# Kernel tuning notes

Hardware: AMD Instinct MI355X
Metric: run time of the kernel (lower is better)

Reference implementation:

```python
import jax, jax.numpy as jnp
import numpy as np

H, C = 4, 64            # heads, channels per head (graph_hidden_channels)
GHC = H * C             # concat width = 256
FIN = 32                # num_node_features
NHID = 256
NOUT = 256
NEG_SLOPE = 0.2         # PyG GATConv default negative_slope


def gat_conv(x, src, dst, n, W, a_src, a_dst, bias):
    # x: [N, Fin], W: [Fin, H*C], a_src/a_dst: [H, C], bias: [H*C]
    h = (x @ W).reshape(n, H, C)                       # [N,H,C]
    s = (h * a_src).sum(-1)                            # [N,H] src logits
    d = (h * a_dst).sum(-1)                            # [N,H] dst logits
    e = jax.nn.leaky_relu(s[src] + d[dst], NEG_SLOPE)  # [E,H]
    m = jax.ops.segment_max(e, dst, num_segments=n)    # segment softmax (stable)
    ex = jnp.exp(e - m[dst])
    denom = jax.ops.segment_sum(ex, dst, num_segments=n)
    alpha = ex / jnp.maximum(denom[dst], 1e-16)        # [E,H]
    msg = h[src] * alpha[:, :, None]                   # [E,H,C]
    out = jax.ops.segment_sum(msg, dst, num_segments=n)
    return out.reshape(n, GHC) + bias


def setup_inputs() -> dict:
    key = jax.random.key(0)
    ks = jax.random.split(key, 32)
    N, E, G = 50000, 800000, 256
    inp = {
        'x': jax.random.normal(ks[0], (N, FIN), dtype=jnp.float32),
        'edge_index': jax.random.randint(ks[1], (2, E), 0, N, dtype=jnp.int32),
        'batch': jnp.sort(jax.random.randint(ks[2], (N,), 0, G, dtype=jnp.int32)),
        'num_graphs': G,
    }
    def p(k, shape):
        return jax.random.normal(k, shape, dtype=jnp.float32) * 0.05
    # three GATConv layers + head linears
    ins = [FIN, C, C]
    i = 3
    for l, fin in enumerate(ins, start=1):
        inp[f'W{l}'] = p(ks[i], (fin, GHC)); i += 1
        inp[f'a{l}s'] = p(ks[i], (H, C)); i += 1
        inp[f'a{l}d'] = p(ks[i], (H, C)); i += 1
        inp[f'b{l}'] = p(ks[i], (GHC,)); i += 1
        inp[f'hl{l}_w'] = p(ks[i], (GHC, C)); i += 1
        inp[f'hl{l}_b'] = p(ks[i], (C,)); i += 1
    inp['mh1_w'] = p(ks[i], (C, NHID)); i += 1
    inp['mh1_b'] = p(ks[i], (NHID,)); i += 1
    inp['mh2_w'] = p(ks[i], (NHID, NOUT)); i += 1
    inp['mh2_b'] = p(ks[i], (NOUT,))
    return inp


def reference(x, edge_index, batch, num_graphs,
              W1, a1s, a1d, b1, hl1_w, hl1_b,
              W2, a2s, a2d, b2, hl2_w, hl2_b,
              W3, a3s, a3d, b3, hl3_w, hl3_b,
              mh1_w, mh1_b, mh2_w, mh2_b):
    n = x.shape[0]
    loops = jnp.arange(n, dtype=edge_index.dtype)  # PyG add_self_loops=True
    src = jnp.concatenate([edge_index[0], loops])
    dst = jnp.concatenate([edge_index[1], loops])

    h = gat_conv(x, src, dst, n, W1, a1s, a1d, b1)
    h = jax.nn.relu(h @ hl1_w + hl1_b)
    h = gat_conv(h, src, dst, n, W2, a2s, a2d, b2)
    h = jax.nn.relu(h @ hl2_w + hl2_b)
    h = gat_conv(h, src, dst, n, W3, a3s, a3d, b3)
    h = h @ hl3_w + hl3_b                      # no relu before pooling (as in source)

    sums = jax.ops.segment_sum(h, batch, num_segments=num_graphs)
    cnt = jax.ops.segment_sum(jnp.ones((n,), h.dtype), batch, num_segments=num_graphs)
    g = sums / jnp.maximum(cnt, 1.0)[:, None]  # global_mean_pool

    g = jax.nn.relu(g @ mh1_w + mh1_b)
    return g @ mh2_w + mh2_b
```

## Files before the change

kernel.cpp:

```cpp
#include <hip/hip_runtime.h>
#include <hip/hip_bf16.h>
#include <hip/hip_fp16.h>
#include <math.h>

#define HD 4
#define CH 64
#define GHC 256
#define NEG 0.2f
#define CHUNK 4096
#define BCAP 16384

#define WAVE_SYNC() do { __builtin_amdgcn_wave_barrier(); \
                         asm volatile("s_waitcnt lgkmcnt(0)" ::: "memory"); } while (0)

typedef _Float16 f16x8 __attribute__((ext_vector_type(8)));
typedef float f32x4 __attribute__((ext_vector_type(4)));

__device__ __forceinline__ float wsum32(float v){
  #pragma unroll
  for (int o = 16; o > 0; o >>= 1) v += __shfl_xor(v, o);
  return v;
}

__global__ __launch_bounds__(256)
void bin_stage(const int* __restrict__ ei, int E, int N,
               int* __restrict__ bres, unsigned* __restrict__ pairs)
{
  __shared__ unsigned staged[CHUNK];
  __shared__ unsigned short bkt[CHUNK];
  __shared__ int cnts[256], loff[256], gpos[256];
  const int t = threadIdx.x;
  const int tot = E + N;
  const int cbase = blockIdx.x * CHUNK;
  if (cbase >= tot) return;

  cnts[t] = 0;
  __syncthreads();

  unsigned myp[CHUNK / 256];
  int myb[CHUNK / 256], myr[CHUNK / 256];
  #pragma unroll
  for (int j = 0; j < CHUNK / 256; j++){
    int i = cbase + t + j * 256;
    myb[j] = -1;
    if (i < tot){
      int src, dst;
      if (i < E){ src = ei[i]; dst = ei[E + i]; }
      else { src = dst = i - E; }
      myb[j] = dst >> 8;
      myp[j] = (unsigned)src | ((unsigned)dst << 16);
      myr[j] = atomicAdd(&cnts[myb[j]], 1);
    }
  }
  __syncthreads();

  int v = cnts[t];
  loff[t] = v;
  __syncthreads();
  for (int o = 1; o < 256; o <<= 1){
    int tv = (t >= o) ? loff[t - o] : 0;
    __syncthreads();
    loff[t] += tv;
    __syncthreads();
  }
  int excl = loff[t] - v;
  __syncthreads();
  loff[t] = excl;
  __syncthreads();

  #pragma unroll
  for (int j = 0; j < CHUNK / 256; j++){
    if (myb[j] >= 0){
      int slot = loff[myb[j]] + myr[j];
      staged[slot] = myp[j];
      bkt[slot] = (unsigned short)myb[j];
    }
  }
  if (v > 0) gpos[t] = atomicAdd(&bres[t], v);
  __syncthreads();

  int total = min(CHUNK, tot - cbase);
  for (int i = t; i < total; i += 256){
    int b = bkt[i];
    int addr = b * BCAP + gpos[b] + (i - loff[b]);
    pairs[addr] = staged[i];
  }
}

__global__ __launch_bounds__(256)
void build_csr(const unsigned* __restrict__ pairs, const int* __restrict__ bres,
               int N, int Etot, int* __restrict__ offs, unsigned short* __restrict__ csr)
{
  __shared__ int dcnt[256], doff[256], bscan[256];
  const int b = blockIdx.x, t = threadIdx.x;
  int bv = bres[t];
  bscan[t] = bv;
  __syncthreads();
  for (int o = 1; o < 256; o <<= 1){
    int tv = (t >= o) ? bscan[t - o] : 0;
    __syncthreads();
    bscan[t] += tv;
    __syncthreads();
  }
  const int beg = bscan[b] - bres[b];
  const int cnt = bres[b];
  const unsigned* pb = pairs + (size_t)b * BCAP;
  dcnt[t] = 0;
  __syncthreads();
  for (int i = t; i < cnt; i += 256)
    atomicAdd(&dcnt[(pb[i] >> 16) & 255], 1);
  __syncthreads();
  int v = dcnt[t];
  doff[t] = v;
  __syncthreads();
  for (int o = 1; o < 256; o <<= 1){
    int tv = (t >= o) ? doff[t - o] : 0;
    __syncthreads();
    doff[t] += tv;
    __syncthreads();
  }
  int excl = doff[t] - v;
  __syncthreads();
  doff[t] = excl;
  __syncthreads();
  int node = (b << 8) + t;
  if (node < N) offs[node] = beg + doff[t];
  if (b == 0 && t == 0) offs[N] = Etot;
  dcnt[t] = 0;
  __syncthreads();
  for (int i = t; i < cnt; i += 256){
    unsigned pr = pb[i];
    int l = (pr >> 16) & 255;
    int pos = beg + doff[l] + atomicAdd(&dcnt[l], 1);
    csr[pos] = (unsigned short)(pr & 0xFFFF);
  }
}

__global__ __launch_bounds__(256)
void fuse_all(const float* __restrict__ W1, const float* __restrict__ a1s,
              const float* __restrict__ a1d, const float* __restrict__ b1,
              const float* __restrict__ h1w, const float* __restrict__ h1b,
              const float* __restrict__ W2, const float* __restrict__ a2s,
              const float* __restrict__ a2d, const float* __restrict__ b2,
              const float* __restrict__ h2w, const float* __restrict__ h2b,
              const float* __restrict__ W3, const float* __restrict__ a3s,
              const float* __restrict__ a3d, const float* __restrict__ b3,
              const float* __restrict__ h3w, const float* __restrict__ h3b,
              __half* __restrict__ Wpk1, float* __restrict__ Psd1, float* __restrict__ cb1,
              __half* __restrict__ Wpk2, __half* __restrict__ Ppk2, float* __restrict__ cb2,
              float* __restrict__ Wcp3, __half* __restrict__ Ppk3, float* __restrict__ cb3,
              const int* __restrict__ batch, int N, int G, int* __restrict__ bnd)
{
  const int blk = blockIdx.x, t = threadIdx.x;
  if (blk >= 163){
    int g = (blk - 163) * 256 + t;
    if (g > G) return;
    if (g == G){ bnd[G] = N; return; }
    int lo = 0, hi = N;
    while (lo < hi){ int mid = (lo + hi) >> 1; if (batch[mid] < g) lo = mid + 1; else hi = mid; }
    bnd[g] = lo;
    return;
  }
  const float *W, *as, *ad, *bl, *hlw, *hlb;
  float *cb;
  int FIN, b, layer;
  if (blk < 33){
    W = W1; as = a1s; ad = a1d; bl = b1; hlw = h1w; hlb = h1b;
    cb = cb1; FIN = 32; b = blk; layer = 1;
  } else if (blk < 98){
    W = W2; as = a2s; ad = a2d; bl = b2; hlw = h2w; hlb = h2b;
    cb = cb2; FIN = 64; b = blk - 33; layer = 2;
  } else {
    W = W3; as = a3s; ad = a3d; bl = b3; hlw = h3w; hlb = h3b;
    cb = cb3; FIN = 64; b = blk - 98; layer = 3;
  }
  if (b < FIN){
    const int c = t >> 2, h = t & 3;
    const float* wrow = W + b * GHC + h * 64;
    float acc = 0.f;
    #pragma unroll 8
    for (int j = 0; j < 64; j++)
      acc += wrow[j] * hlw[(h * 64 + j) * CH + c];
    const int k = h * FIN + b;
    if (layer == 3){
      Wcp3[k * CH + c] = acc;
    } else {
      int ks = k >> 5, nt = c >> 4;
      int lane = (((k & 31) >> 3) << 4) | (c & 15);
      int idx = ((ks * 4 + nt) * 64 + lane) * 8 + (k & 7);
      __half* Wpk = (layer == 1) ? Wpk1 : Wpk2;
      Wpk[idx] = __float2half(acc);
    }
    if (t < 8){
      const int hh = t & 3;
      const float* a = (t < 4) ? as : ad;
      const float* wr2 = W + b * GHC + hh * 64;
      float p = 0.f;
      #pragma unroll 8
      for (int j = 0; j < 64; j++) p += wr2[j] * a[hh * 64 + j];
      if (layer == 1){
        Psd1[b * 8 + t] = p;
      } else {
        int kk = b;
        int ks = kk >> 5;
        int lane = (((kk & 31) >> 3) << 4) | t;
        int idx = (ks * 64 + lane) * 8 + (kk & 7);
        __half* Ppk = (layer == 2) ? Ppk2 : Ppk3;
        Ppk[idx] = __float2half(p);
      }
    }
  } else if (t < CH){
    float acc = hlb[t];
    for (int j = 0; j < GHC; j++) acc += bl[j] * hlw[j * CH + t];
    cb[t] = acc;
  }
}

__global__ __launch_bounds__(256)
void logits_from_x(const float* __restrict__ x, const float* __restrict__ Psd,
                   float* __restrict__ s_log, float* __restrict__ d_log,
                   __half* __restrict__ xh0, int N)
{
  int idx = blockIdx.x * 256 + threadIdx.x;
  int node = idx >> 3, q = idx & 7;
  if (node >= N) return;
  const float* xr = x + (size_t)node * 32;
  float v = 0.f;
  #pragma unroll 8
  for (int k = 0; k < 32; k++) v += xr[k] * Psd[k * 8 + q];
  if (q < 4){
    s_log[node * 4 + q] = v;
    __half2 h0 = __floats2half2_rn(xr[q*8+0], xr[q*8+1]);
    __half2 h1 = __floats2half2_rn(xr[q*8+2], xr[q*8+3]);
    __half2 h2 = __floats2half2_rn(xr[q*8+4], xr[q*8+5]);
    __half2 h3 = __floats2half2_rn(xr[q*8+6], xr[q*8+7]);
    uint4 u;
    u.x = *reinterpret_cast<const unsigned*>(&h0);
    u.y = *reinterpret_cast<const unsigned*>(&h1);
    u.z = *reinterpret_cast<const unsigned*>(&h2);
    u.w = *reinterpret_cast<const unsigned*>(&h3);
    *reinterpret_cast<uint4*>(xh0 + (size_t)node * 32 + q * 8) = u;
  } else {
    d_log[node * 4 + (q - 4)] = v;
  }
}

template<int F, int ZW>
__global__ __launch_bounds__(512)
void gat_layer_fused(const __half* __restrict__ xin, const float* __restrict__ s_in,
                     const float* __restrict__ d_in_, const int* __restrict__ off,
                     const unsigned short* __restrict__ csr,
                     const __half* __restrict__ Wpk, const float* __restrict__ cb,
                     const __half* __restrict__ Ppk,
                     __half* __restrict__ xo, float* __restrict__ s_out,
                     float* __restrict__ d_out_, int N)
{
  constexpr int ZP = ZW + 8;
  __shared__ float4 qa[8][2][32];
  __shared__ int    qs[8][2][32];
  __shared__ __half z_lds[16][ZP];
  __shared__ float  outs[16][68];
  __shared__ float  cbs[64];
  const int tid  = threadIdx.x;
  const int wv   = tid >> 6;
  const int lane = tid & 63;
  const int half = lane >> 5;
  const int l32  = lane & 31;
  const int n0 = blockIdx.x * 16;
  const int n = n0 + wv * 2 + half;
  const bool valid = n < N;
  if (tid < 64) cbs[tid] = cb[tid];

  int beg = 0, deg = 0;
  if (valid){ beg = off[n]; deg = off[n + 1] - beg; }

  float d4[4] = {0.f, 0.f, 0.f, 0.f};
  if (valid){
    float4 d4v = reinterpret_cast<const float4*>(d_in_)[n];
    d4[0] = d4v.x; d4[1] = d4v.y; d4[2] = d4v.z; d4[3] = d4v.w;
  }

  float den[4], ex[4];
  int s = 0;
  {
    const bool act = valid && (l32 < deg);
    if (act){
      s = csr[beg + l32];
      float4 sl = reinterpret_cast<const float4*>(s_in)[s];
      float t[4] = {sl.x, sl.y, sl.z, sl.w};
      #pragma unroll
      for (int i = 0; i < 4; i++){
        float u = t[i] + d4[i]; u = (u >= 0.f) ? u : NEG * u;
        ex[i] = __expf(u);
      }
    } else {
      #pragma unroll
      for (int i = 0; i < 4; i++) ex[i] = 0.f;
    }
    #pragma unroll
    for (int i = 0; i < 4; i++) den[i] = wsum32(ex[i]);
  }
  for (int base = 32; base < deg; base += 32){
    const int k = base + l32;
    float e2[4] = {0.f, 0.f, 0.f, 0.f};
    if (k < deg){
      int s2 = csr[beg + k];
      float4 sl = reinterpret_cast<const float4*>(s_in)[s2];
      float t[4] = {sl.x, sl.y, sl.z, sl.w};
      #pragma unroll
      for (int i = 0; i < 4; i++){
        float u = t[i] + d4[i]; u = (u >= 0.f) ? u : NEG * u;
        e2[i] = __expf(u);
      }
    }
    #pragma unroll
    for (int i = 0; i < 4; i++) den[i] += wsum32(e2[i]);
  }

  float dninv[4];
  #pragma unroll
  for (int i = 0; i < 4; i++) dninv[i] = 1.f / fmaxf(den[i], 1e-16f);

  float a0[4] = {0.f,0.f,0.f,0.f};
  float a1[4] = {0.f,0.f,0.f,0.f};
  const float4* qap = qa[wv][half];
  const int*    qsp = qs[wv][half];

  auto accum = [&](int cnt){
    int cntR = (cnt + 3) & ~3;
    if (F == 64){
      const __half* xb = xin + 2 * l32;
      for (int e0 = 0; e0 < cntR; e0 += 4){
        float4 al[4]; int sv[4]; unsigned uv[4];
        #pragma unroll
        for (int j = 0; j < 4; j++){ al[j] = qap[e0 + j]; sv[j] = qsp[e0 + j]; }
        #pragma unroll
        for (int j = 0; j < 4; j++)
          uv[j] = *reinterpret_cast<const unsigned*>(xb + sv[j] * 64);
        #pragma unroll
        for (int j = 0; j < 4; j++){
          float2 f = __half22float2(*reinterpret_cast<const __half2*>(&uv[j]));
          a0[0] += al[j].x * f.x; a1[0] += al[j].x * f.y;
          a0[1] += al[j].y * f.x; a1[1] += al[j].y * f.y;
          a0[2] += al[j].z * f.x; a1[2] += al[j].z * f.y;
          a0[3] += al[j].w * f.x; a1[3] += al[j].w * f.y;
        }
      }
    } else {
      const __half* xb = xin + l32;
      for (int e0 = 0; e0 < cntR; e0 += 4){
        float4 al[4]; int sv[4]; __half hv[4];
        #pragma unroll
        for (int j = 0; j < 4; j++){ al[j] = qap[e0 + j]; sv[j] = qsp[e0 + j]; }
        #pragma unroll
        for (int j = 0; j < 4; j++)
          hv[j] = xb[sv[j] * 32];
        #pragma unroll
        for (int j = 0; j < 4; j++){
          float xv = __half2float(hv[j]);
          a0[0] += al[j].x * xv;
          a0[1] += al[j].y * xv;
          a0[2] += al[j].z * xv;
          a0[3] += al[j].w * xv;
        }
      }
    }
  };

  if (deg <= 32){
    qa[wv][half][l32] = make_float4(ex[0] * dninv[0], ex[1] * dninv[1],
                                    ex[2] * dninv[2], ex[3] * dninv[3]);
    qs[wv][half][l32] = s;
    WAVE_SYNC();
    accum(deg);
  } else {
    for (int base = 0; base < deg; base += 32){
      const int k = base + l32;
      int s2 = 0; float al[4] = {0.f, 0.f, 0.f, 0.f};
      if (k < deg){
        s2 = csr[beg + k];
        float4 sl = reinterpret_cast<const float4*>(s_in)[s2];
        float t[4] = {sl.x, sl.y, sl.z, sl.w};
        #pragma unroll
        for (int i = 0; i < 4; i++){
          float u = t[i] + d4[i]; u = (u >= 0.f) ? u : NEG * u;
          al[i] = __expf(u) * dninv[i];
        }
      }
      qa[wv][half][l32] = make_float4(al[0], al[1], al[2], al[3]);
      qs[wv][half][l32] = s2;
      WAVE_SYNC();
      accum(min(32, deg - base));
      WAVE_SYNC();
    }
  }

  {
    const int r = wv * 2 + half;
    if (F == 64){
      #pragma unroll
      for (int h = 0; h < 4; h++){
        __half2 hv = __floats2half2_rn(a0[h], a1[h]);
        *reinterpret_cast<unsigned*>(&z_lds[r][h * 64 + 2 * l32]) =
            *reinterpret_cast<const unsigned*>(&hv);
      }
    } else {
      #pragma unroll
      for (int h = 0; h < 4; h++)
        z_lds[r][h * 32 + l32] = __float2half(a0[h]);
    }
  }
  __syncthreads();

  const int row = lane & 15, kg = lane >> 4;
  if (wv < 4){
    const int nt = wv;
    f32x4 acc = {0.f,0.f,0.f,0.f};
    const f16x8* wp = reinterpret_cast<const f16x8*>(Wpk) + lane;
    #pragma unroll
    for (int ks = 0; ks < ZW / 32; ks++){
      f16x8 af = *reinterpret_cast<const f16x8*>(&z_lds[row][kg * 8 + ks * 32]);
      acc = __builtin_amdgcn_mfma_f32_16x16x32_f16(af, wp[(ks*4+nt)*64], acc, 0,0,0);
    }
    #pragma unroll
    for (int r = 0; r < 4; r++){
      int rr = kg * 4 + r;
      outs[rr][nt * 16 + row] = fmaxf(acc[r] + cbs[nt * 16 + row], 0.f);
    }
  }
  __syncthreads();

  if (tid < 256){
    int nn = tid >> 4, part = tid & 15;
    int node = n0 + nn;
    if (node < N){
      const float* o = &outs[nn][part * 4];
      __half2 h0 = __floats2half2_rn(o[0], o[1]);
      __half2 h1 = __floats2half2_rn(o[2], o[3]);
      uint2 u;
      u.x = *reinterpret_cast<const unsigned*>(&h0);
      u.y = *reinterpret_cast<const unsigned*>(&h1);
      *reinterpret_cast<uint2*>(xo + (size_t)node * 64 + part * 4) = u;
    }
  }

  if (wv == 4){
    f32x4 lacc = {0.f,0.f,0.f,0.f};
    const f16x8* pp = reinterpret_cast<const f16x8*>(Ppk) + lane;
    #pragma unroll
    for (int ks = 0; ks < 2; ks++){
      f16x8 af;
      #pragma unroll
      for (int j = 0; j < 8; j++) af[j] = (_Float16)outs[row][ks * 32 + kg * 8 + j];
      lacc = __builtin_amdgcn_mfma_f32_16x16x32_f16(af, pp[ks * 64], lacc, 0,0,0);
    }
    if (row < 8){
      float* dst = (row < 4) ? s_out : d_out_;
      int q = row & 3;
      #pragma unroll
      for (int r = 0; r < 4; r++){
        int node = n0 + kg * 4 + r;
        if (node < N) dst[node * 4 + q] = lacc[r];
      }
    }
  }
}

template<int F>
__global__ __launch_bounds__(256)
void gat_aggregate_z(const __half* __restrict__ xin, const float* __restrict__ s_log,
                     const float* __restrict__ d_log, const int* __restrict__ off,
                     const unsigned short* __restrict__ csr, __half* __restrict__ z, int N)
{
  __shared__ float4 qa[4][2][32];
  __shared__ int    qs[4][2][32];
  const int wv   = threadIdx.x >> 6;
  const int lane = threadIdx.x & 63;
  const int half = lane >> 5;
  const int l32  = lane & 31;
  const int n = blockIdx.x * 8 + wv * 2 + half;
  const bool valid = n < N;

  int beg = 0, deg = 0;
  if (valid){ beg = off[n]; deg = off[n + 1] - beg; }

  float d4[4] = {0.f, 0.f, 0.f, 0.f};
  if (valid){
    float4 d4v = reinterpret_cast<const float4*>(d_log)[n];
    d4[0] = d4v.x; d4[1] = d4v.y; d4[2] = d4v.z; d4[3] = d4v.w;
  }

  float den[4], ex[4];
  int s = 0;
  {
    const bool act = valid && (l32 < deg);
    if (act){
      s = csr[beg + l32];
      float4 sl = reinterpret_cast<const float4*>(s_log)[s];
      float t[4] = {sl.x, sl.y, sl.z, sl.w};
      #pragma unroll
      for (int i = 0; i < 4; i++){
        float u = t[i] + d4[i]; u = (u >= 0.f) ? u : NEG * u;
        ex[i] = __expf(u);
      }
    } else {
      #pragma unroll
      for (int i = 0; i < 4; i++) ex[i] = 0.f;
    }
    #pragma unroll
    for (int i = 0; i < 4; i++) den[i] = wsum32(ex[i]);
  }
  for (int base = 32; base < deg; base += 32){
    const int k = base + l32;
    float e2[4] = {0.f, 0.f, 0.f, 0.f};
    if (k < deg){
      int s2 = csr[beg + k];
      float4 sl = reinterpret_cast<const float4*>(s_log)[s2];
      float t[4] = {sl.x, sl.y, sl.z, sl.w};
      #pragma unroll
      for (int i = 0; i < 4; i++){
        float u = t[i] + d4[i]; u = (u >= 0.f) ? u : NEG * u;
        e2[i] = __expf(u);
      }
    }
    #pragma unroll
    for (int i = 0; i < 4; i++) den[i] += wsum32(e2[i]);
  }

  float dninv[4];
  #pragma unroll
  for (int i = 0; i < 4; i++) dninv[i] = 1.f / fmaxf(den[i], 1e-16f);

  float a0[4] = {0.f,0.f,0.f,0.f};
  float a1[4] = {0.f,0.f,0.f,0.f};
  const float4* qap = qa[wv][half];
  const int*    qsp = qs[wv][half];

  auto accum = [&](int cnt){
    int cntR = (cnt + 3) & ~3;
    const __half* xb = xin + 2 * l32;
    for (int e0 = 0; e0 < cntR; e0 += 4){
      float4 al[4]; int sv[4]; unsigned uv[4];
      #pragma unroll
      for (int j = 0; j < 4; j++){ al[j] = qap[e0 + j]; sv[j] = qsp[e0 + j]; }
      #pragma unroll
      for (int j = 0; j < 4; j++)
        uv[j] = *reinterpret_cast<const unsigned*>(xb + sv[j] * 64);
      #pragma unroll
      for (int j = 0; j < 4; j++){
        float2 f = __half22float2(*reinterpret_cast<const __half2*>(&uv[j]));
        a0[0] += al[j].x * f.x; a1[0] += al[j].x * f.y;
        a0[1] += al[j].y * f.x; a1[1] += al[j].y * f.y;
        a0[2] += al[j].z * f.x; a1[2] += al[j].z * f.y;
        a0[3] += al[j].w * f.x; a1[3] += al[j].w * f.y;
      }
    }
  };

  if (deg <= 32){
    qa[wv][half][l32] = make_float4(ex[0] * dninv[0], ex[1] * dninv[1],
                                    ex[2] * dninv[2], ex[3] * dninv[3]);
    qs[wv][half][l32] = s;
    WAVE_SYNC();
    accum(deg);
  } else {
    for (int base = 0; base < deg; base += 32){
      const int k = base + l32;
      int s2 = 0; float al[4] = {0.f, 0.f, 0.f, 0.f};
      if (k < deg){
        s2 = csr[beg + k];
        float4 sl = reinterpret_cast<const float4*>(s_log)[s2];
        float t[4] = {sl.x, sl.y, sl.z, sl.w};
        #pragma unroll
        for (int i = 0; i < 4; i++){
          float u = t[i] + d4[i]; u = (u >= 0.f) ? u : NEG * u;
          al[i] = __expf(u) * dninv[i];
        }
      }
      qa[wv][half][l32] = make_float4(al[0], al[1], al[2], al[3]);
      qs[wv][half][l32] = s2;
      WAVE_SYNC();
      accum(min(32, deg - base));
      WAVE_SYNC();
    }
  }

  if (valid){
    const size_t zb = (size_t)n * 256 + 2 * l32;
    #pragma unroll
    for (int h = 0; h < 4; h++){
      __half2 hv = __floats2half2_rn(a0[h], a1[h]);
      *reinterpret_cast<unsigned*>(z + zb + h * 64) =
          *reinterpret_cast<const unsigned*>(&hv);
    }
  }
}

__global__ __launch_bounds__(256)
void pool_partial(const __half* __restrict__ z3, const int* __restrict__ bnd,
                  float* __restrict__ psum)
{
  const int blk = blockIdx.x, tid = threadIdx.x;
  const int g = blk >> 2, part = blk & 3;
  const int s = bnd[g], e = bnd[g + 1];
  const int cp = tid & 127, rp = tid >> 7;
  float ax = 0.f, ay = 0.f;
  for (int n = s + part + 4 * rp; n < e; n += 8){
    __half2 hv = *reinterpret_cast<const __half2*>(z3 + (size_t)n * 256 + 2 * cp);
    float2 f = __half22float2(hv);
    ax += f.x; ay += f.y;
  }
  __shared__ float shx[2][128], shy[2][128];
  shx[rp][cp] = ax; shy[rp][cp] = ay;
  __syncthreads();
  if (tid < 128){
    psum[(size_t)blk * 256 + 2 * tid]     = shx[0][tid] + shx[1][tid];
    psum[(size_t)blk * 256 + 2 * tid + 1] = shy[0][tid] + shy[1][tid];
  }
}

__global__ __launch_bounds__(256)
void head_mlp(const float* __restrict__ psum, const int* __restrict__ bnd,
              const float* __restrict__ Wcp3, const float* __restrict__ cb3,
              const float* __restrict__ m1w, const float* __restrict__ m1b,
              const float* __restrict__ m2w, const float* __restrict__ m2b,
              float* __restrict__ out)
{
  const int g = blockIdx.x, tid = threadIdx.x;
  const float cnt = (float)max(bnd[g + 1] - bnd[g], 1);
  __shared__ float zbar[256];
  const float* pb = psum + (size_t)g * 1024;
  zbar[tid] = (pb[tid] + pb[256 + tid] + pb[512 + tid] + pb[768 + tid]) / cnt;
  __syncthreads();
  const int c = tid & 63, part = tid >> 6;
  float tp = 0.f;
  #pragma unroll 8
  for (int k = part * 64; k < part * 64 + 64; k++) tp += zbar[k] * Wcp3[k * 64 + c];
  __shared__ float tsh[4][64];
  tsh[part][c] = tp;
  __syncthreads();
  __shared__ float tvec[64];
  if (tid < 64)
    tvec[tid] = tsh[0][tid] + tsh[1][tid] + tsh[2][tid] + tsh[3][tid] + cb3[tid];
  __syncthreads();
  float a = m1b[tid];
  #pragma unroll 8
  for (int cc = 0; cc < 64; cc++) a += tvec[cc] * m1w[cc * 256 + tid];
  __shared__ float g1row[256];
  g1row[tid] = fmaxf(a, 0.f);
  __syncthreads();
  float o = m2b[tid];
  #pragma unroll 8
  for (int k = 0; k < 256; k++) o += g1row[k] * m2w[k * 256 + tid];
  out[g * 256 + tid] = o;
}

extern "C" void kernel_launch(void* const* d_in, const int* in_sizes, int n_in,
                              void* d_out, int out_size, void* d_ws, size_t ws_size,
                              hipStream_t stream)
{
  const float* x     = (const float*)d_in[0];
  const int*   ei    = (const int*)d_in[1];
  const int*   batch = (const int*)d_in[2];
  const float* W1  = (const float*)d_in[4];
  const float* a1s = (const float*)d_in[5];
  const float* a1d = (const float*)d_in[6];
  const float* b1  = (const float*)d_in[7];
  const float* h1w = (const float*)d_in[8];
  const float* h1b = (const float*)d_in[9];
  const float* W2  = (const float*)d_in[10];
  const float* a2s = (const float*)d_in[11];
  const float* a2d = (const float*)d_in[12];
  const float* b2  = (const float*)d_in[13];
  const float* h2w = (const float*)d_in[14];
  const float* h2b = (const float*)d_in[15];
  const float* W3  = (const float*)d_in[16];
  const float* a3s = (const float*)d_in[17];
  const float* a3d = (const float*)d_in[18];
  const float* b3  = (const float*)d_in[19];
  const float* h3w = (const float*)d_in[20];
  const float* h3b = (const float*)d_in[21];
  const float* m1w = (const float*)d_in[22];
  const float* m1b = (const float*)d_in[23];
  const float* m2w = (const float*)d_in[24];
  const float* m2b = (const float*)d_in[25];

  const int N = in_sizes[0] / 32;
  const int E = in_sizes[1] / 2;
  const int G = out_size / 256;
  const int Etot = E + N;
  const int nbuck = (N + 255) >> 8;

  char* p = (char*)d_ws;
  auto alloc = [&](size_t bytes) -> void* {
    void* r = (void*)p;
    p += ((bytes + 255) / 256) * 256;
    return r;
  };
  __half* zbuf   = (__half*)alloc((size_t)N * GHC * 2);
  __half* xh0    = (__half*)alloc((size_t)N * 32 * 2);
  __half* xh1    = (__half*)alloc((size_t)N * CH * 2);
  __half* xh2    = (__half*)alloc((size_t)N * CH * 2);
  float* s_logA  = (float*)alloc((size_t)N * HD * 4);
  float* d_logA  = (float*)alloc((size_t)N * HD * 4);
  float* s_logB  = (float*)alloc((size_t)N * HD * 4);
  float* d_logB  = (float*)alloc((size_t)N * HD * 4);
  int*   offs    = (int*)alloc((size_t)(N + 1) * 4);
  unsigned short* csr = (unsigned short*)alloc((size_t)Etot * 2);
  unsigned* pairs = (unsigned*)alloc((size_t)nbuck * BCAP * 4);
  int*    bres   = (int*)alloc(256 * 4);
  __half* Ppk2   = (__half*)alloc(1024 * 2);
  __half* Ppk3   = (__half*)alloc(1024 * 2);
  int*   bnd     = (int*)alloc((size_t)(G + 1) * 4);
  float* psum    = (float*)alloc((size_t)G * 4 * 256 * 4);
  float* Wcp3    = (float*)alloc(256 * 64 * 4);
  float* Psd1    = (float*)alloc(32 * 8 * 4);
  float* cb1     = (float*)alloc(64 * 4);
  float* cb2     = (float*)alloc(64 * 4);
  float* cb3     = (float*)alloc(64 * 4);
  __half* Wpk1   = (__half*)alloc(128 * 64 * 2);
  __half* Wpk2   = (__half*)alloc(256 * 64 * 2);

  hipMemsetAsync(bres, 0, 5120, stream);

  const int cb_blocks = (Etot + CHUNK - 1) / CHUNK;
  bin_stage<<<cb_blocks, 256, 0, stream>>>(ei, E, N, bres, pairs);
  build_csr<<<nbuck, 256, 0, stream>>>(pairs, bres, N, Etot, offs, csr);

  const int fb = 163 + (G + 256) / 256;
  fuse_all<<<fb, 256, 0, stream>>>(W1, a1s, a1d, b1, h1w, h1b,
                                   W2, a2s, a2d, b2, h2w, h2b,
                                   W3, a3s, a3d, b3, h3w, h3b,
                                   Wpk1, Psd1, cb1, Wpk2, Ppk2, cb2, Wcp3, Ppk3, cb3,
                                   batch, N, G, bnd);

  logits_from_x<<<((size_t)N * 8 + 255) / 256, 256, 0, stream>>>(x, Psd1, s_logA, d_logA, xh0, N);

  const int fgrid = (N + 15) / 16;
  gat_layer_fused<32, 128><<<fgrid, 512, 0, stream>>>(xh0, s_logA, d_logA, offs, csr,
                                                      Wpk1, cb1, Ppk2, xh1, s_logB, d_logB, N);
  gat_layer_fused<64, 256><<<fgrid, 512, 0, stream>>>(xh1, s_logB, d_logB, offs, csr,
                                                      Wpk2, cb2, Ppk3, xh2, s_logA, d_logA, N);

  const int ab = (N + 7) / 8;
  gat_aggregate_z<64><<<ab, 256, 0, stream>>>(xh2, s_logA, d_logA, offs, csr, zbuf, N);

  pool_partial<<<G * 4, 256, 0, stream>>>(zbuf, bnd, psum);
  head_mlp<<<G, 256, 0, stream>>>(psum, bnd, Wcp3, cb3, m1w, m1b, m2w, m2b, (float*)d_out);
}
```

Before: 161.7 us.

## Sort nodes by in-degree so aggregation blocks process similar-degree nodes

Adds a degree histogram in build_csr and a new perm_scatter kernel that buckets nodes by in-degree into a permutation array. The GAT layer kernels and the final aggregation then read their node ids through this permutation, so the nodes sharing a wave or block have similar degree. The aim is to cut load imbalance and idle lanes when degrees vary within a wave. The cost is an extra kernel launch, global atomics, and scattered, less coalesced writes of per-node outputs. Neighbour locality is also lost.

```diff
diff --git a/kernel.cpp b/kernel.cpp
--- a/kernel.cpp
+++ b/kernel.cpp
@@ -89,7 +89,8 @@
 
 __global__ __launch_bounds__(256)
 void build_csr(const unsigned* __restrict__ pairs, const int* __restrict__ bres,
-               int N, int Etot, int* __restrict__ offs, unsigned short* __restrict__ csr)
+               int N, int Etot, int* __restrict__ offs, unsigned short* __restrict__ csr,
+               int* __restrict__ ghist)
 {
   __shared__ int dcnt[256], doff[256], bscan[256];
   const int b = blockIdx.x, t = threadIdx.x;
@@ -124,7 +125,10 @@
   doff[t] = excl;
   __syncthreads();
   int node = (b << 8) + t;
-  if (node < N) offs[node] = beg + doff[t];
+  if (node < N){
+    offs[node] = beg + doff[t];
+    atomicAdd(&ghist[min(v, 255)], 1);
+  }
   if (b == 0 && t == 0) offs[N] = Etot;
   dcnt[t] = 0;
   __syncthreads();
@@ -133,6 +137,33 @@
     int l = (pr >> 16) & 255;
     int pos = beg + doff[l] + atomicAdd(&dcnt[l], 1);
     csr[pos] = (unsigned short)(pr & 0xFFFF);
+  }
+}
+
+__global__ __launch_bounds__(256)
+void perm_scatter(const int* __restrict__ offs, const int* __restrict__ ghist,
+                  int* __restrict__ gbincnt, int* __restrict__ perm, int N)
+{
+  __shared__ int sc[256];
+  const int t = threadIdx.x;
+  int v = ghist[t];
+  sc[t] = v;
+  __syncthreads();
+  for (int o = 1; o < 256; o <<= 1){
+    int tv = (t >= o) ? sc[t - o] : 0;
+    __syncthreads();
+    sc[t] += tv;
+    __syncthreads();
+  }
+  __shared__ int base[256];
+  base[t] = sc[t] - v;
+  __syncthreads();
+  int node = blockIdx.x * 256 + t;
+  if (node < N){
+    int deg = offs[node + 1] - offs[node];
+    int bin = min(deg, 255);
+    int pos = base[bin] + atomicAdd(&gbincnt[bin], 1);
+    perm[pos] = node;
   }
 }
 
@@ -249,7 +280,7 @@
 __global__ __launch_bounds__(512)
 void gat_layer_fused(const __half* __restrict__ xin, const float* __restrict__ s_in,
                      const float* __restrict__ d_in_, const int* __restrict__ off,
-                     const unsigned short* __restrict__ csr,
+                     const unsigned short* __restrict__ csr, const int* __restrict__ perm,
                      const __half* __restrict__ Wpk, const float* __restrict__ cb,
                      const __half* __restrict__ Ppk,
                      __half* __restrict__ xo, float* __restrict__ s_out,
@@ -261,15 +292,20 @@
   __shared__ __half z_lds[16][ZP];
   __shared__ float  outs[16][68];
   __shared__ float  cbs[64];
+  __shared__ int    pnode[16];
   const int tid  = threadIdx.x;
   const int wv   = tid >> 6;
   const int lane = tid & 63;
   const int half = lane >> 5;
   const int l32  = lane & 31;
   const int n0 = blockIdx.x * 16;
-  const int n = n0 + wv * 2 + half;
-  const bool valid = n < N;
   if (tid < 64) cbs[tid] = cb[tid];
+  if (tid < 16) pnode[tid] = (n0 + tid < N) ? perm[n0 + tid] : 0;
+  __syncthreads();
+
+  const int li = wv * 2 + half;
+  const bool valid = (n0 + li) < N;
+  const int n = pnode[li];
 
   int beg = 0, deg = 0;
   if (valid){ beg = off[n]; deg = off[n + 1] - beg; }
@@ -396,7 +432,7 @@
   }
 
   {
-    const int r = wv * 2 + half;
+    const int r = li;
     if (F == 64){
       #pragma unroll
       for (int h = 0; h < 4; h++){
@@ -432,8 +468,8 @@
 
   if (tid < 256){
     int nn = tid >> 4, part = tid & 15;
-    int node = n0 + nn;
-    if (node < N){
+    if (n0 + nn < N){
+      int node = pnode[nn];
       const float* o = &outs[nn][part * 4];
       __half2 h0 = __floats2half2_rn(o[0], o[1]);
       __half2 h1 = __floats2half2_rn(o[2], o[3]);
@@ -459,18 +495,20 @@
       int q = row & 3;
       #pragma unroll
       for (int r = 0; r < 4; r++){
-        int node = n0 + kg * 4 + r;
-        if (node < N) dst[node * 4 + q] = lacc[r];
-      }
-    }
-  }
-}
-
-template<int F>
+        if (n0 + kg * 4 + r < N){
+          int node = pnode[kg * 4 + r];
+          dst[node * 4 + q] = lacc[r];
+        }
+      }
+    }
+  }
+}
+
 __global__ __launch_bounds__(256)
-void gat_aggregate_z(const __half* __restrict__ xin, const float* __restrict__ s_log,
-                     const float* __restrict__ d_log, const int* __restrict__ off,
-                     const unsigned short* __restrict__ csr, __half* __restrict__ z, int N)
+void gat_aggregate_z3(const __half* __restrict__ xin, const float* __restrict__ s_log,
+                      const float* __restrict__ d_log, const int* __restrict__ off,
+                      const unsigned short* __restrict__ csr, const int* __restrict__ perm,
+                      __half* __restrict__ z, int N)
 {
   __shared__ float4 qa[4][2][32];
   __shared__ int    qs[4][2][32];
@@ -478,8 +516,9 @@
   const int lane = threadIdx.x & 63;
   const int half = lane >> 5;
   const int l32  = lane & 31;
-  const int n = blockIdx.x * 8 + wv * 2 + half;
-  const bool valid = n < N;
+  const int idx = blockIdx.x * 8 + wv * 2 + half;
+  const bool valid = idx < N;
+  const int n = valid ? perm[idx] : 0;
 
   int beg = 0, deg = 0;
   if (valid){ beg = off[n]; deg = off[n + 1] - beg; }
@@ -706,11 +745,14 @@
   float* s_logB  = (float*)alloc((size_t)N * HD * 4);
   float* d_logB  = (float*)alloc((size_t)N * HD * 4);
   int*   offs    = (int*)alloc((size_t)(N + 1) * 4);
+  int*   perm    = (int*)alloc((size_t)N * 4);
   unsigned short* csr = (unsigned short*)alloc((size_t)Etot * 2);
   unsigned* pairs = (unsigned*)alloc((size_t)nbuck * BCAP * 4);
   int*    bres   = (int*)alloc(256 * 4);
   __half* Ppk2   = (__half*)alloc(1024 * 2);
   __half* Ppk3   = (__half*)alloc(1024 * 2);
+  int*    ghist  = (int*)alloc(256 * 4);
+  int*    gbincnt= (int*)alloc(256 * 4);
   int*   bnd     = (int*)alloc((size_t)(G + 1) * 4);
   float* psum    = (float*)alloc((size_t)G * 4 * 256 * 4);
   float* Wcp3    = (float*)alloc(256 * 64 * 4);
@@ -721,11 +763,12 @@
   __half* Wpk1   = (__half*)alloc(128 * 64 * 2);
   __half* Wpk2   = (__half*)alloc(256 * 64 * 2);
 
-  hipMemsetAsync(bres, 0, 5120, stream);
+  hipMemsetAsync(bres, 0, 7168, stream);
 
   const int cb_blocks = (Etot + CHUNK - 1) / CHUNK;
   bin_stage<<<cb_blocks, 256, 0, stream>>>(ei, E, N, bres, pairs);
-  build_csr<<<nbuck, 256, 0, stream>>>(pairs, bres, N, Etot, offs, csr);
+  build_csr<<<nbuck, 256, 0, stream>>>(pairs, bres, N, Etot, offs, csr, ghist);
+  perm_scatter<<<nbuck, 256, 0, stream>>>(offs, ghist, gbincnt, perm, N);
 
   const int fb = 163 + (G + 256) / 256;
   fuse_all<<<fb, 256, 0, stream>>>(W1, a1s, a1d, b1, h1w, h1b,
@@ -737,13 +780,13 @@
   logits_from_x<<<((size_t)N * 8 + 255) / 256, 256, 0, stream>>>(x, Psd1, s_logA, d_logA, xh0, N);
 
   const int fgrid = (N + 15) / 16;
-  gat_layer_fused<32, 128><<<fgrid, 512, 0, stream>>>(xh0, s_logA, d_logA, offs, csr,
+  gat_layer_fused<32, 128><<<fgrid, 512, 0, stream>>>(xh0, s_logA, d_logA, offs, csr, perm,
                                                       Wpk1, cb1, Ppk2, xh1, s_logB, d_logB, N);
-  gat_layer_fused<64, 256><<<fgrid, 512, 0, stream>>>(xh1, s_logB, d_logB, offs, csr,
+  gat_layer_fused<64, 256><<<fgrid, 512, 0, stream>>>(xh1, s_logB, d_logB, offs, csr, perm,
                                                       Wpk2, cb2, Ppk3, xh2, s_logA, d_logA, N);
 
   const int ab = (N + 7) / 8;
-  gat_aggregate_z<64><<<ab, 256, 0, stream>>>(xh2, s_logA, d_logA, offs, csr, zbuf, N);
+  gat_aggregate_z3<<<ab, 256, 0, stream>>>(xh2, s_logA, d_logA, offs, csr, perm, zbuf, N);
 
   pool_partial<<<G * 4, 256, 0, stream>>>(zbuf, bnd, psum);
   head_mlp<<<G, 256, 0, stream>>>(psum, bnd, Wcp3, cb3, m1w, m1b, m2w, m2b, (float*)d_out);
```

After: 447.3 us. 2.77x slower.
